# Performance work log

Measured on AMD Instinct MI355X. Metric: run time of the kernel, lower is better.

## Reference

```python
import jax, jax.numpy as jnp
import numpy as np

B, T, H, P = 512, 256, 256, 14  # batch, seq_len, hidden_size, predict_seq


def _lstm_layer(x_tbf, w_ih, w_hh, b_ih, b_hh):
    """One LSTM layer. x_tbf: [T, B, F]. Returns outputs [T, B, H].
    PyTorch gate order: i, f, g, o."""
    # Precompute input contribution for all timesteps: [T, B, 4H]
    pre = jnp.einsum('tbf,gf->tbg', x_tbf, w_ih) + b_ih + b_hh
    h0 = jnp.zeros((x_tbf.shape[1], w_hh.shape[1]), dtype=x_tbf.dtype)
    c0 = jnp.zeros_like(h0)

    def step(carry, pre_t):
        h, c = carry
        gates = pre_t + h @ w_hh.T                      # [B, 4H]
        i, f, g, o = jnp.split(gates, 4, axis=-1)
        i = jax.nn.sigmoid(i)
        f = jax.nn.sigmoid(f)
        g = jnp.tanh(g)
        o = jax.nn.sigmoid(o)
        c = f * c + i * g
        h = o * jnp.tanh(c)
        return (h, c), h

    _, ys = jax.lax.scan(step, (h0, c0), pre)
    return ys  # [T, B, H]


def setup_inputs() -> dict:
    key = jax.random.key(0)
    ks = jax.random.split(key, 11)
    s = 1.0 / np.sqrt(H)  # torch LSTM/Linear default init scale
    return {
        'x':     jax.random.normal(ks[0], (B, T, 1), dtype=jnp.float32),
        'w_ih0': jax.random.uniform(ks[1], (4 * H, 1), jnp.float32, -s, s),
        'w_hh0': jax.random.uniform(ks[2], (4 * H, H), jnp.float32, -s, s),
        'b_ih0': jax.random.uniform(ks[3], (4 * H,), jnp.float32, -s, s),
        'b_hh0': jax.random.uniform(ks[4], (4 * H,), jnp.float32, -s, s),
        'w_ih1': jax.random.uniform(ks[5], (4 * H, H), jnp.float32, -s, s),
        'w_hh1': jax.random.uniform(ks[6], (4 * H, H), jnp.float32, -s, s),
        'b_ih1': jax.random.uniform(ks[7], (4 * H,), jnp.float32, -s, s),
        'b_hh1': jax.random.uniform(ks[8], (4 * H,), jnp.float32, -s, s),
        'w_lin': jax.random.uniform(ks[9], (P, H), jnp.float32, -s, s),
        'b_lin': jax.random.uniform(ks[10], (P,), jnp.float32, -s, s),
    }


def reference(x, w_ih0, w_hh0, b_ih0, b_hh0, w_ih1, w_hh1, b_ih1, b_hh1,
              w_lin, b_lin):
    xt = jnp.transpose(x, (1, 0, 2))                 # [T, B, 1]
    h1 = _lstm_layer(xt, w_ih0, w_hh0, b_ih0, b_hh0)  # [T, B, H]
    h2 = _lstm_layer(h1, w_ih1, w_hh1, b_ih1, b_hh1)  # [T, B, H]
    last = h2[-1]                                     # [B, H] == x[:, -1, :]
    return last @ w_lin.T + b_lin                     # [B, P]
```

## Files before the change

kernel.cpp:

```cpp
#include <hip/hip_runtime.h>

constexpr int Bz = 512;
constexpr int Tz = 256;
constexpr int Hz = 256;
constexpr int Pz = 14;
constexpr int GB = 32;
constexpr int GS = 8;
constexpr int BT = 16;
constexpr int KP = 264;
constexpr int XS = 260;

typedef short s8v __attribute__((ext_vector_type(8)));
typedef float f4v __attribute__((ext_vector_type(4)));
typedef unsigned long long u64;

__device__ __forceinline__ short f2bf(float f) {
  unsigned u = __float_as_uint(f);
  u = (u + 0x7fffu + ((u >> 16) & 1u)) >> 16;
  return (short)u;
}
__device__ __forceinline__ float bf2f(short s) {
  return __uint_as_float(((unsigned)(unsigned short)s) << 16);
}
__device__ __forceinline__ float sigm(float v) {
  return __builtin_amdgcn_rcpf(1.0f + __builtin_amdgcn_exp2f(-1.442695041f * v));
}
__device__ __forceinline__ float tanh_f(float v) {
  return 1.0f - 2.0f * __builtin_amdgcn_rcpf(__builtin_amdgcn_exp2f(2.885390082f * v) + 1.0f);
}

__device__ __forceinline__ u64 llc_load64(const u64* p) {
  return __hip_atomic_load(p, __ATOMIC_RELAXED, __HIP_MEMORY_SCOPE_AGENT);
}
__device__ __forceinline__ unsigned llc_load32(const unsigned* p) {
  return __hip_atomic_load(p, __ATOMIC_RELAXED, __HIP_MEMORY_SCOPE_AGENT);
}
__device__ __forceinline__ void llc_store32(unsigned* p, unsigned v) {
  __hip_atomic_store(p, v, __ATOMIC_RELAXED, __HIP_MEMORY_SCOPE_AGENT);
}
__device__ __forceinline__ void llc_store64(u64* p, u64 v) {
  __hip_atomic_store(p, v, __ATOMIC_RELAXED, __HIP_MEMORY_SCOPE_AGENT);
}

__global__ void __launch_bounds__(256, 1)
lstm2(const float* __restrict__ x,
      const float* __restrict__ w_ih0, const float* __restrict__ w_hh0,
      const float* __restrict__ b_ih0, const float* __restrict__ b_hh0,
      const float* __restrict__ w_ih1, const float* __restrict__ w_hh1,
      const float* __restrict__ b_ih1, const float* __restrict__ b_hh1,
      const float* __restrict__ w_lin, const float* __restrict__ b_lin,
      float* __restrict__ out,
      u64* __restrict__ hg, unsigned* __restrict__ flags)
{
  const int blk  = blockIdx.x;
  const int g    = blk >> 3;
  const int sl   = blk & 7;
  const int tid  = threadIdx.x;
  const int w    = tid >> 6;
  const int lane = tid & 63;
  const int q    = lane >> 4;
  const int l15  = lane & 15;
  const int gbase = g * BT;

  extern __shared__ char smem_raw[];
  short* h0s = (short*)smem_raw;
  short* h1s = h0s + BT * KP;
  float* xls = (float*)(h1s + BT * KP);
  float* wls = xls + BT * XS;

  s8v Wf[3][2][8];
  {
    const float* wsrc[3] = {w_hh0, w_ih1, w_hh1};
    #pragma unroll
    for (int mat = 0; mat < 3; ++mat) {
      #pragma unroll
      for (int mti = 0; mti < 2; ++mti) {
        int rr = (w + mti * 4) * 16 + l15;
        int grow = (rr & 3) * Hz + sl * 32 + (rr >> 2);
        const float* p = wsrc[mat] + (size_t)grow * Hz;
        #pragma unroll
        for (int kt = 0; kt < 8; ++kt) {
          s8v f;
          #pragma unroll
          for (int j = 0; j < 8; ++j) {
            int ktrue = kt * 32 + q * 4 + (j >> 1) + 16 * (j & 1);
            f[j] = f2bf(p[ktrue]);
          }
          Wf[mat][mti][kt] = f;
        }
      }
    }
  }
  const int uA = w * 4 + q, uB = 16 + w * 4 + q;
  float wihA[4], wihB[4], b0A[4], b0B[4], b1A[4], b1B[4];
  #pragma unroll
  for (int r = 0; r < 4; ++r) {
    int ga_ = r * Hz + sl * 32 + uA;
    int gb_ = r * Hz + sl * 32 + uB;
    wihA[r] = w_ih0[ga_];              wihB[r] = w_ih0[gb_];
    b0A[r]  = b_ih0[ga_] + b_hh0[ga_]; b0B[r]  = b_ih0[gb_] + b_hh0[gb_];
    b1A[r]  = b_ih1[ga_] + b_hh1[ga_]; b1B[r]  = b_ih1[gb_] + b_hh1[gb_];
  }
  float c0A = 0.f, c0B = 0.f, c1A = 0.f, c1B = 0.f;

  for (int i = tid; i < BT * (Tz / 4); i += 256) {
    int b = i >> 6, c4 = i & 63;
    f4v v = *(const f4v*)(x + (size_t)(gbase + b) * Tz + c4 * 4);
    *(f4v*)(xls + b * XS + c4 * 4) = v;
  }
  if (sl == 0) {
    for (int i = tid; i < Pz * Hz; i += 256) {
      int p = i >> 8, kpos = i & 255;
      int sl2 = kpos >> 5, w2 = (kpos >> 3) & 3, q2 = (kpos >> 1) & 3, jj = kpos & 1;
      wls[i] = w_lin[p * Hz + sl2 * 32 + w2 * 4 + q2 + 16 * jj];
    }
  }

  const unsigned* myflags = flags + g * 32 + (lane & 7);
  unsigned* myflag = flags + g * 32 + sl;

  for (int s = 0; s <= Tz; ++s) {
    if (w == 0) {
      const unsigned expd = (unsigned)s;
      unsigned f = llc_load32(myflags);
      while (__ballot(f >= expd) != ~0ull) {
        __builtin_amdgcn_s_sleep(1);
        f = llc_load32(myflags);
      }
    }
    __syncthreads();

    {
      const u64* sp = hg + (size_t)((s + 1) & 1) * 65536;
      u64 r[8];
      #pragma unroll
      for (int k = 0; k < 4; ++k) {
        int i = tid + k * 256;
        int c = i & 1, b = (i >> 1) & 15, slw = i >> 5;
        size_t gi = ((size_t)slw * Bz + gbase + b) * 4 + 2 * c;
        r[2 * k]     = llc_load64(sp + gi);
        r[2 * k + 1] = llc_load64(sp + gi + 1);
      }
      #pragma unroll
      for (int k = 0; k < 4; ++k) {
        int i = tid + k * 256;
        int c = i & 1, b = (i >> 1) & 15, slw = i >> 5;
        u64 lo = r[2 * k], hi = r[2 * k + 1];
        *(u64*)(h0s + b * KP + slw * 8 + c * 4) =
            (u64)(unsigned)lo | ((u64)(unsigned)hi << 32);
        *(u64*)(h1s + b * KP + slw * 8 + c * 4) =
            (lo >> 32) | ((hi >> 32) << 32);
      }
    }
    __syncthreads();

    f4v a0A = {0.f,0.f,0.f,0.f}, a0B = {0.f,0.f,0.f,0.f};
    f4v a1A = {0.f,0.f,0.f,0.f}, a1B = {0.f,0.f,0.f,0.f};
    const short* H0f = h0s + l15 * KP + q * 8;
    const short* H1f = h1s + l15 * KP + q * 8;
    #pragma unroll
    for (int kt = 0; kt < 8; ++kt) {
      s8v h0v = *(const s8v*)(H0f + kt * 32);
      s8v h1v = *(const s8v*)(H1f + kt * 32);
      a0A = __builtin_amdgcn_mfma_f32_16x16x32_bf16(Wf[0][0][kt], h0v, a0A, 0, 0, 0);
      a0B = __builtin_amdgcn_mfma_f32_16x16x32_bf16(Wf[0][1][kt], h0v, a0B, 0, 0, 0);
      a1A = __builtin_amdgcn_mfma_f32_16x16x32_bf16(Wf[1][0][kt], h0v, a1A, 0, 0, 0);
      a1B = __builtin_amdgcn_mfma_f32_16x16x32_bf16(Wf[1][1][kt], h0v, a1B, 0, 0, 0);
      a1A = __builtin_amdgcn_mfma_f32_16x16x32_bf16(Wf[2][0][kt], h1v, a1A, 0, 0, 0);
      a1B = __builtin_amdgcn_mfma_f32_16x16x32_bf16(Wf[2][1][kt], h1v, a1B, 0, 0, 0);
    }

    unsigned pk0 = 0, pk1 = 0;
    if (s < Tz) {
      float xv = xls[l15 * XS + s];
      float iA = sigm  (a0A[0] + xv * wihA[0] + b0A[0]);
      float fA = sigm  (a0A[1] + xv * wihA[1] + b0A[1]);
      float gA = tanh_f(a0A[2] + xv * wihA[2] + b0A[2]);
      float oA = sigm  (a0A[3] + xv * wihA[3] + b0A[3]);
      c0A = fA * c0A + iA * gA;
      float iB = sigm  (a0B[0] + xv * wihB[0] + b0B[0]);
      float fB = sigm  (a0B[1] + xv * wihB[1] + b0B[1]);
      float gB = tanh_f(a0B[2] + xv * wihB[2] + b0B[2]);
      float oB = sigm  (a0B[3] + xv * wihB[3] + b0B[3]);
      c0B = fB * c0B + iB * gB;
      pk0 = (unsigned)(unsigned short)f2bf(oA * tanh_f(c0A))
          | ((unsigned)(unsigned short)f2bf(oB * tanh_f(c0B)) << 16);
    }
    if (s >= 1) {
      float iA = sigm  (a1A[0] + b1A[0]);
      float fA = sigm  (a1A[1] + b1A[1]);
      float gA = tanh_f(a1A[2] + b1A[2]);
      float oA = sigm  (a1A[3] + b1A[3]);
      c1A = fA * c1A + iA * gA;
      float iB = sigm  (a1B[0] + b1B[0]);
      float fB = sigm  (a1B[1] + b1B[1]);
      float gB = tanh_f(a1B[2] + b1B[2]);
      float oB = sigm  (a1B[3] + b1B[3]);
      c1B = fB * c1B + iB * gB;
      pk1 = (unsigned)(unsigned short)f2bf(oA * tanh_f(c1A))
          | ((unsigned)(unsigned short)f2bf(oB * tanh_f(c1B)) << 16);
    }

    {
      size_t base = (size_t)(sl * 4 + w) * 2048 + (size_t)(gbase + l15) * 4 + q;
      llc_store64(hg + (size_t)(s & 1) * 65536 + base,
                  (u64)pk0 | ((u64)pk1 << 32));
    }

    __syncthreads();
    if (tid == 0)
      llc_store32(myflag, (unsigned)(s + 1));
  }

  if (sl == 0) {
    {
      const unsigned expd = (unsigned)(Tz + 1);
      unsigned f = llc_load32(myflags);
      while (__ballot(f >= expd) != ~0ull) {
        __builtin_amdgcn_s_sleep(1);
        f = llc_load32(myflags);
      }
    }
    const u64* sp = hg + (size_t)(Tz & 1) * 65536;
    for (int k = 0; k < 4; ++k) {
      int i = tid + k * 256;
      int c = i & 1, b = (i >> 1) & 15, slw = i >> 5;
      size_t gi = ((size_t)slw * Bz + gbase + b) * 4 + 2 * c;
      u64 lo = llc_load64(sp + gi);
      u64 hi = llc_load64(sp + gi + 1);
      *(u64*)(h0s + b * KP + slw * 8 + c * 4) = (lo >> 32) | ((hi >> 32) << 32);
    }
    __syncthreads();
    for (int i = tid; i < BT * Pz; i += 256) {
      int b = i / Pz, p = i - b * Pz;
      const float* wr = wls + p * Hz;
      float acc = b_lin[p];
      for (int kk = 0; kk < Hz; ++kk)
        acc += bf2f(h0s[b * KP + kk]) * wr[kk];
      out[(gbase + b) * Pz + p] = acc;
    }
  }
}

extern "C" void kernel_launch(void* const* d_in, const int* in_sizes, int n_in,
                              void* d_out, int out_size, void* d_ws, size_t ws_size,
                              hipStream_t stream) {
  const float* x     = (const float*)d_in[0];
  const float* w_ih0 = (const float*)d_in[1];
  const float* w_hh0 = (const float*)d_in[2];
  const float* b_ih0 = (const float*)d_in[3];
  const float* b_hh0 = (const float*)d_in[4];
  const float* w_ih1 = (const float*)d_in[5];
  const float* w_hh1 = (const float*)d_in[6];
  const float* b_ih1 = (const float*)d_in[7];
  const float* b_hh1 = (const float*)d_in[8];
  const float* w_lin = (const float*)d_in[9];
  const float* b_lin = (const float*)d_in[10];
  float* out = (float*)d_out;

  unsigned char* ws = (unsigned char*)d_ws;
  u64* hg         = (u64*)ws;
  unsigned* flags = (unsigned*)(ws + (1 << 20));
  hipMemsetAsync(d_ws, 0, (1 << 20) + 4096, stream);

  size_t lds_bytes = (size_t)(2 * BT) * KP * 2
                   + (size_t)(BT * XS) * 4
                   + (size_t)(Pz * Hz) * 4;
  hipFuncSetAttribute((const void*)lstm2,
                      hipFuncAttributeMaxDynamicSharedMemorySize, (int)lds_bytes);
  lstm2<<<GB * GS, 256, lds_bytes, stream>>>(x, w_ih0, w_hh0, b_ih0, b_hh0,
                                             w_ih1, w_hh1, b_ih1, b_hh1,
                                             w_lin, b_lin, out, hg, flags);
}
```

Before: 727.5 us.

## Split each batch group across 4 blocks of 512 threads instead of 8

Halves the number of blocks cooperating on each 16-row batch group, from 8 to 4, and doubles threads per block to 512 so each block owns 64 hidden units. Weight fragment indexing, hidden-state exchange layout, flag polling and the final linear weight permutation are remapped to match. The aim is to cut the cross-block flag synchronisation and global hidden-state exchange per timestep, at the cost of more work per block and higher register pressure at 512 threads.

```diff
diff --git a/kernel.cpp b/kernel.cpp
--- a/kernel.cpp
+++ b/kernel.cpp
@@ -5,10 +5,11 @@
 constexpr int Hz = 256;
 constexpr int Pz = 14;
 constexpr int GB = 32;
-constexpr int GS = 8;
+constexpr int GS = 4;
 constexpr int BT = 16;
 constexpr int KP = 264;
 constexpr int XS = 260;
+constexpr int THR = 512;
 
 typedef short s8v __attribute__((ext_vector_type(8)));
 typedef float f4v __attribute__((ext_vector_type(4)));
@@ -42,7 +43,7 @@
   __hip_atomic_store(p, v, __ATOMIC_RELAXED, __HIP_MEMORY_SCOPE_AGENT);
 }
 
-__global__ void __launch_bounds__(256, 1)
+__global__ void __launch_bounds__(512, 1)
 lstm2(const float* __restrict__ x,
       const float* __restrict__ w_ih0, const float* __restrict__ w_hh0,
       const float* __restrict__ b_ih0, const float* __restrict__ b_hh0,
@@ -53,8 +54,8 @@
       u64* __restrict__ hg, unsigned* __restrict__ flags)
 {
   const int blk  = blockIdx.x;
-  const int g    = blk >> 3;
-  const int sl   = blk & 7;
+  const int g    = blk >> 2;
+  const int sl   = blk & 3;
   const int tid  = threadIdx.x;
   const int w    = tid >> 6;
   const int lane = tid & 63;
@@ -75,15 +76,16 @@
     for (int mat = 0; mat < 3; ++mat) {
       #pragma unroll
       for (int mti = 0; mti < 2; ++mti) {
-        int rr = (w + mti * 4) * 16 + l15;
-        int grow = (rr & 3) * Hz + sl * 32 + (rr >> 2);
+        int rr = (w + mti * 8) * 16 + l15;
+        int grow = (rr & 3) * Hz + sl * 64 + (rr >> 2);
         const float* p = wsrc[mat] + (size_t)grow * Hz;
         #pragma unroll
         for (int kt = 0; kt < 8; ++kt) {
           s8v f;
           #pragma unroll
           for (int j = 0; j < 8; ++j) {
-            int ktrue = kt * 32 + q * 4 + (j >> 1) + 16 * (j & 1);
+            int xk = kt * 4 + q;
+            int ktrue = (xk >> 3) * 64 + (xk & 7) * 4 + (j >> 1) + 32 * (j & 1);
             f[j] = f2bf(p[ktrue]);
           }
           Wf[mat][mti][kt] = f;
@@ -91,32 +93,34 @@
       }
     }
   }
-  const int uA = w * 4 + q, uB = 16 + w * 4 + q;
+  const int uA = sl * 64 + w * 4 + q, uB = uA + 32;
   float wihA[4], wihB[4], b0A[4], b0B[4], b1A[4], b1B[4];
   #pragma unroll
   for (int r = 0; r < 4; ++r) {
-    int ga_ = r * Hz + sl * 32 + uA;
-    int gb_ = r * Hz + sl * 32 + uB;
+    int ga_ = r * Hz + uA;
+    int gb_ = r * Hz + uB;
     wihA[r] = w_ih0[ga_];              wihB[r] = w_ih0[gb_];
     b0A[r]  = b_ih0[ga_] + b_hh0[ga_]; b0B[r]  = b_ih0[gb_] + b_hh0[gb_];
     b1A[r]  = b_ih1[ga_] + b_hh1[ga_]; b1B[r]  = b_ih1[gb_] + b_hh1[gb_];
   }
   float c0A = 0.f, c0B = 0.f, c1A = 0.f, c1B = 0.f;
 
-  for (int i = tid; i < BT * (Tz / 4); i += 256) {
+  for (int i = tid; i < BT * (Tz / 4); i += THR) {
     int b = i >> 6, c4 = i & 63;
     f4v v = *(const f4v*)(x + (size_t)(gbase + b) * Tz + c4 * 4);
     *(f4v*)(xls + b * XS + c4 * 4) = v;
   }
   if (sl == 0) {
-    for (int i = tid; i < Pz * Hz; i += 256) {
+    for (int i = tid; i < Pz * Hz; i += THR) {
       int p = i >> 8, kpos = i & 255;
-      int sl2 = kpos >> 5, w2 = (kpos >> 3) & 3, q2 = (kpos >> 1) & 3, jj = kpos & 1;
-      wls[i] = w_lin[p * Hz + sl2 * 32 + w2 * 4 + q2 + 16 * jj];
-    }
-  }
-
-  const unsigned* myflags = flags + g * 32 + (lane & 7);
+      int slw2 = kpos >> 3, inner = kpos & 7;
+      int q2 = inner >> 1, j2 = inner & 1;
+      int ktrue = (slw2 >> 3) * 64 + (slw2 & 7) * 4 + q2 + 32 * j2;
+      wls[i] = w_lin[p * Hz + ktrue];
+    }
+  }
+
+  const unsigned* myflags = flags + g * 32 + (lane & 3);
   unsigned* myflag = flags + g * 32 + sl;
 
   for (int s = 0; s <= Tz; ++s) {
@@ -132,18 +136,18 @@
 
     {
       const u64* sp = hg + (size_t)((s + 1) & 1) * 65536;
-      u64 r[8];
+      u64 r[4];
       #pragma unroll
-      for (int k = 0; k < 4; ++k) {
-        int i = tid + k * 256;
+      for (int k = 0; k < 2; ++k) {
+        int i = tid + k * THR;
         int c = i & 1, b = (i >> 1) & 15, slw = i >> 5;
         size_t gi = ((size_t)slw * Bz + gbase + b) * 4 + 2 * c;
         r[2 * k]     = llc_load64(sp + gi);
         r[2 * k + 1] = llc_load64(sp + gi + 1);
       }
       #pragma unroll
-      for (int k = 0; k < 4; ++k) {
-        int i = tid + k * 256;
+      for (int k = 0; k < 2; ++k) {
+        int i = tid + k * THR;
         int c = i & 1, b = (i >> 1) & 15, slw = i >> 5;
         u64 lo = r[2 * k], hi = r[2 * k + 1];
         *(u64*)(h0s + b * KP + slw * 8 + c * 4) =
@@ -202,7 +206,7 @@
     }
 
     {
-      size_t base = (size_t)(sl * 4 + w) * 2048 + (size_t)(gbase + l15) * 4 + q;
+      size_t base = (size_t)(sl * 8 + w) * 2048 + (size_t)(gbase + l15) * 4 + q;
       llc_store64(hg + (size_t)(s & 1) * 65536 + base,
                   (u64)pk0 | ((u64)pk1 << 32));
     }
@@ -222,8 +226,8 @@
       }
     }
     const u64* sp = hg + (size_t)(Tz & 1) * 65536;
-    for (int k = 0; k < 4; ++k) {
-      int i = tid + k * 256;
+    for (int k = 0; k < 2; ++k) {
+      int i = tid + k * THR;
       int c = i & 1, b = (i >> 1) & 15, slw = i >> 5;
       size_t gi = ((size_t)slw * Bz + gbase + b) * 4 + 2 * c;
       u64 lo = llc_load64(sp + gi);
@@ -231,7 +235,7 @@
       *(u64*)(h0s + b * KP + slw * 8 + c * 4) = (lo >> 32) | ((hi >> 32) << 32);
     }
     __syncthreads();
-    for (int i = tid; i < BT * Pz; i += 256) {
+    for (int i = tid; i < BT * Pz; i += THR) {
       int b = i / Pz, p = i - b * Pz;
       const float* wr = wls + p * Hz;
       float acc = b_lin[p];
@@ -268,7 +272,7 @@
                    + (size_t)(Pz * Hz) * 4;
   hipFuncSetAttribute((const void*)lstm2,
                       hipFuncAttributeMaxDynamicSharedMemorySize, (int)lds_bytes);
-  lstm2<<<GB * GS, 256, lds_bytes, stream>>>(x, w_ih0, w_hh0, b_ih0, b_hh0,
+  lstm2<<<GB * GS, THR, lds_bytes, stream>>>(x, w_ih0, w_hh0, b_ih0, b_hh0,
                                              w_ih1, w_hh1, b_ih1, b_hh1,
                                              w_lin, b_lin, out, hg, flags);
 }
```

Result: slower. 1.098 ms (+51.0%).

## Replace end-of-step block barrier with per-wave atomic counters and double-buffered LDS

Applied to the files above, without the earlier changes.

Drops the trailing __syncthreads and single-thread flag store at the end of each timestep. Each wave now drains its own stores and atomically increments a per-block counter, and waiters expect 4 increments per step. The hidden-state LDS staging is double-buffered by step parity, so a fast wave cannot overwrite data a slower wave is still reading. The intent is to cut one block-wide barrier per step on the latency-bound recurrent path, at the cost of 4x more atomic traffic to the flag lines and twice the LDS for h staging.

```diff
diff --git a/kernel.cpp b/kernel.cpp
--- a/kernel.cpp
+++ b/kernel.cpp
@@ -9,6 +9,7 @@
 constexpr int BT = 16;
 constexpr int KP = 264;
 constexpr int XS = 260;
+constexpr int HBsz = BT * KP;
 
 typedef short s8v __attribute__((ext_vector_type(8)));
 typedef float f4v __attribute__((ext_vector_type(4)));
@@ -34,9 +35,6 @@
 }
 __device__ __forceinline__ unsigned llc_load32(const unsigned* p) {
   return __hip_atomic_load(p, __ATOMIC_RELAXED, __HIP_MEMORY_SCOPE_AGENT);
-}
-__device__ __forceinline__ void llc_store32(unsigned* p, unsigned v) {
-  __hip_atomic_store(p, v, __ATOMIC_RELAXED, __HIP_MEMORY_SCOPE_AGENT);
 }
 __device__ __forceinline__ void llc_store64(u64* p, u64 v) {
   __hip_atomic_store(p, v, __ATOMIC_RELAXED, __HIP_MEMORY_SCOPE_AGENT);
@@ -63,9 +61,8 @@
   const int gbase = g * BT;
 
   extern __shared__ char smem_raw[];
-  short* h0s = (short*)smem_raw;
-  short* h1s = h0s + BT * KP;
-  float* xls = (float*)(h1s + BT * KP);
+  short* hstage = (short*)smem_raw;
+  float* xls = (float*)(hstage + 4 * HBsz);
   float* wls = xls + BT * XS;
 
   s8v Wf[3][2][8];
@@ -116,39 +113,44 @@
     }
   }
 
-  const unsigned* myflags = flags + g * 32 + (lane & 7);
-  unsigned* myflag = flags + g * 32 + sl;
+  const unsigned* myctrs = flags + g * 16 + (lane & 7);
+  unsigned* myctr = flags + g * 16 + sl;
+
+  int cc[4], bb[4], ss[4];
+  #pragma unroll
+  for (int k = 0; k < 4; ++k) {
+    int i = tid + k * 256;
+    cc[k] = i & 1; bb[k] = (i >> 1) & 15; ss[k] = i >> 5;
+  }
 
   for (int s = 0; s <= Tz; ++s) {
     if (w == 0) {
-      const unsigned expd = (unsigned)s;
-      unsigned f = llc_load32(myflags);
+      const unsigned expd = 4u * (unsigned)s;
+      unsigned f = llc_load32(myctrs);
       while (__ballot(f >= expd) != ~0ull) {
         __builtin_amdgcn_s_sleep(1);
-        f = llc_load32(myflags);
+        f = llc_load32(myctrs);
       }
     }
     __syncthreads();
 
+    short* hb0 = hstage + (s & 1) * (2 * HBsz);
+    short* hb1 = hb0 + HBsz;
     {
       const u64* sp = hg + (size_t)((s + 1) & 1) * 65536;
       u64 r[8];
       #pragma unroll
       for (int k = 0; k < 4; ++k) {
-        int i = tid + k * 256;
-        int c = i & 1, b = (i >> 1) & 15, slw = i >> 5;
-        size_t gi = ((size_t)slw * Bz + gbase + b) * 4 + 2 * c;
+        size_t gi = ((size_t)ss[k] * Bz + gbase + bb[k]) * 4 + 2 * cc[k];
         r[2 * k]     = llc_load64(sp + gi);
         r[2 * k + 1] = llc_load64(sp + gi + 1);
       }
       #pragma unroll
       for (int k = 0; k < 4; ++k) {
-        int i = tid + k * 256;
-        int c = i & 1, b = (i >> 1) & 15, slw = i >> 5;
         u64 lo = r[2 * k], hi = r[2 * k + 1];
-        *(u64*)(h0s + b * KP + slw * 8 + c * 4) =
+        *(u64*)(hb0 + bb[k] * KP + ss[k] * 8 + cc[k] * 4) =
             (u64)(unsigned)lo | ((u64)(unsigned)hi << 32);
-        *(u64*)(h1s + b * KP + slw * 8 + c * 4) =
+        *(u64*)(hb1 + bb[k] * KP + ss[k] * 8 + cc[k] * 4) =
             (lo >> 32) | ((hi >> 32) << 32);
       }
     }
@@ -156,8 +158,8 @@
 
     f4v a0A = {0.f,0.f,0.f,0.f}, a0B = {0.f,0.f,0.f,0.f};
     f4v a1A = {0.f,0.f,0.f,0.f}, a1B = {0.f,0.f,0.f,0.f};
-    const short* H0f = h0s + l15 * KP + q * 8;
-    const short* H1f = h1s + l15 * KP + q * 8;
+    const short* H0f = hb0 + l15 * KP + q * 8;
+    const short* H1f = hb1 + l15 * KP + q * 8;
     #pragma unroll
     for (int kt = 0; kt < 8; ++kt) {
       s8v h0v = *(const s8v*)(H0f + kt * 32);
@@ -207,28 +209,30 @@
                   (u64)pk0 | ((u64)pk1 << 32));
     }
 
-    __syncthreads();
-    if (tid == 0)
-      llc_store32(myflag, (unsigned)(s + 1));
+    asm volatile("s_waitcnt vmcnt(0)" ::: "memory");
+    __builtin_amdgcn_sched_barrier(0);
+    if (lane == 0)
+      __hip_atomic_fetch_add(myctr, 1u, __ATOMIC_RELAXED,
+                             __HIP_MEMORY_SCOPE_AGENT);
   }
 
   if (sl == 0) {
     {
-      const unsigned expd = (unsigned)(Tz + 1);
-      unsigned f = llc_load32(myflags);
+      const unsigned expd = 4u * (unsigned)(Tz + 1);
+      unsigned f = llc_load32(myctrs);
       while (__ballot(f >= expd) != ~0ull) {
         __builtin_amdgcn_s_sleep(1);
-        f = llc_load32(myflags);
-      }
-    }
+        f = llc_load32(myctrs);
+      }
+    }
+    short* hb = hstage + 1 * (2 * HBsz);
     const u64* sp = hg + (size_t)(Tz & 1) * 65536;
     for (int k = 0; k < 4; ++k) {
-      int i = tid + k * 256;
-      int c = i & 1, b = (i >> 1) & 15, slw = i >> 5;
-      size_t gi = ((size_t)slw * Bz + gbase + b) * 4 + 2 * c;
+      size_t gi = ((size_t)ss[k] * Bz + gbase + bb[k]) * 4 + 2 * cc[k];
       u64 lo = llc_load64(sp + gi);
       u64 hi = llc_load64(sp + gi + 1);
-      *(u64*)(h0s + b * KP + slw * 8 + c * 4) = (lo >> 32) | ((hi >> 32) << 32);
+      *(u64*)(hb + bb[k] * KP + ss[k] * 8 + cc[k] * 4) =
+          (lo >> 32) | ((hi >> 32) << 32);
     }
     __syncthreads();
     for (int i = tid; i < BT * Pz; i += 256) {
@@ -236,7 +240,7 @@
       const float* wr = wls + p * Hz;
       float acc = b_lin[p];
       for (int kk = 0; kk < Hz; ++kk)
-        acc += bf2f(h0s[b * KP + kk]) * wr[kk];
+        acc += bf2f(hb[b * KP + kk]) * wr[kk];
       out[(gbase + b) * Pz + p] = acc;
     }
   }
@@ -263,7 +267,7 @@
   unsigned* flags = (unsigned*)(ws + (1 << 20));
   hipMemsetAsync(d_ws, 0, (1 << 20) + 4096, stream);
 
-  size_t lds_bytes = (size_t)(2 * BT) * KP * 2
+  size_t lds_bytes = (size_t)(4 * HBsz) * 2
                    + (size_t)(BT * XS) * 4
                    + (size_t)(Pz * Hz) * 4;
   hipFuncSetAttribute((const void*)lstm2,
```

After: 1.020 ms. 40.2% more time.

## Split LSTM layers into separate producer/consumer block roles with decoupled flags

Applied to the files above, without the earlier changes.

Launches twice as many blocks: role 0 blocks run layer 0 only, role 1 blocks run layer 1 and the final linear. Layer 0 is allowed to run up to three steps ahead using a 4-deep h0 ring buffer, and layer 1 waits on per-step flags. This replaces the lockstep wavefront schedule where each block did both layers per step, and halves the per-block register-resident weights so two blocks can fit per CU. It adds extra flag polling traffic and relies on all 512 blocks being co-resident to avoid deadlock.

```diff
diff --git a/kernel.cpp b/kernel.cpp
--- a/kernel.cpp
+++ b/kernel.cpp
@@ -38,11 +38,8 @@
 __device__ __forceinline__ void llc_store32(unsigned* p, unsigned v) {
   __hip_atomic_store(p, v, __ATOMIC_RELAXED, __HIP_MEMORY_SCOPE_AGENT);
 }
-__device__ __forceinline__ void llc_store64(u64* p, u64 v) {
-  __hip_atomic_store(p, v, __ATOMIC_RELAXED, __HIP_MEMORY_SCOPE_AGENT);
-}
-
-__global__ void __launch_bounds__(256, 1)
+
+__global__ void __launch_bounds__(256, 2)
 lstm2(const float* __restrict__ x,
       const float* __restrict__ w_ih0, const float* __restrict__ w_hh0,
       const float* __restrict__ b_ih0, const float* __restrict__ b_hh0,
@@ -50,11 +47,14 @@
       const float* __restrict__ b_ih1, const float* __restrict__ b_hh1,
       const float* __restrict__ w_lin, const float* __restrict__ b_lin,
       float* __restrict__ out,
-      u64* __restrict__ hg, unsigned* __restrict__ flags)
+      unsigned* __restrict__ h0g, unsigned* __restrict__ h1g,
+      unsigned* __restrict__ flags)
 {
   const int blk  = blockIdx.x;
-  const int g    = blk >> 3;
-  const int sl   = blk & 7;
+  const int role = blk >> 8;
+  const int sub  = blk & 255;
+  const int g    = sub >> 3;
+  const int sl   = sub & 7;
   const int tid  = threadIdx.x;
   const int w    = tid >> 6;
   const int lane = tid & 63;
@@ -68,110 +68,84 @@
   float* xls = (float*)(h1s + BT * KP);
   float* wls = xls + BT * XS;
 
-  s8v Wf[3][2][8];
-  {
-    const float* wsrc[3] = {w_hh0, w_ih1, w_hh1};
+  int cc[4], bb[4], ss[4];
+  #pragma unroll
+  for (int k = 0; k < 4; ++k) {
+    int i = tid + k * 256;
+    cc[k] = i & 1; bb[k] = (i >> 1) & 15; ss[k] = i >> 5;
+  }
+  const size_t stbase = (size_t)(sl * 4 + w) * 2048 + (size_t)(gbase + l15) * 4 + q;
+
+  if (role == 0) {
+    s8v Wf0[2][8];
     #pragma unroll
-    for (int mat = 0; mat < 3; ++mat) {
+    for (int mti = 0; mti < 2; ++mti) {
+      int rr = (w + mti * 4) * 16 + l15;
+      int grow = (rr & 3) * Hz + sl * 32 + (rr >> 2);
+      const float* p = w_hh0 + (size_t)grow * Hz;
       #pragma unroll
-      for (int mti = 0; mti < 2; ++mti) {
-        int rr = (w + mti * 4) * 16 + l15;
-        int grow = (rr & 3) * Hz + sl * 32 + (rr >> 2);
-        const float* p = wsrc[mat] + (size_t)grow * Hz;
-        #pragma unroll
-        for (int kt = 0; kt < 8; ++kt) {
-          s8v f;
-          #pragma unroll
-          for (int j = 0; j < 8; ++j) {
-            int ktrue = kt * 32 + q * 4 + (j >> 1) + 16 * (j & 1);
-            f[j] = f2bf(p[ktrue]);
-          }
-          Wf[mat][mti][kt] = f;
-        }
-      }
-    }
-  }
-  const int uA = w * 4 + q, uB = 16 + w * 4 + q;
-  float wihA[4], wihB[4], b0A[4], b0B[4], b1A[4], b1B[4];
-  #pragma unroll
-  for (int r = 0; r < 4; ++r) {
-    int ga_ = r * Hz + sl * 32 + uA;
-    int gb_ = r * Hz + sl * 32 + uB;
-    wihA[r] = w_ih0[ga_];              wihB[r] = w_ih0[gb_];
-    b0A[r]  = b_ih0[ga_] + b_hh0[ga_]; b0B[r]  = b_ih0[gb_] + b_hh0[gb_];
-    b1A[r]  = b_ih1[ga_] + b_hh1[ga_]; b1B[r]  = b_ih1[gb_] + b_hh1[gb_];
-  }
-  float c0A = 0.f, c0B = 0.f, c1A = 0.f, c1B = 0.f;
-
-  for (int i = tid; i < BT * (Tz / 4); i += 256) {
-    int b = i >> 6, c4 = i & 63;
-    f4v v = *(const f4v*)(x + (size_t)(gbase + b) * Tz + c4 * 4);
-    *(f4v*)(xls + b * XS + c4 * 4) = v;
-  }
-  if (sl == 0) {
-    for (int i = tid; i < Pz * Hz; i += 256) {
-      int p = i >> 8, kpos = i & 255;
-      int sl2 = kpos >> 5, w2 = (kpos >> 3) & 3, q2 = (kpos >> 1) & 3, jj = kpos & 1;
-      wls[i] = w_lin[p * Hz + sl2 * 32 + w2 * 4 + q2 + 16 * jj];
-    }
-  }
-
-  const unsigned* myflags = flags + g * 32 + (lane & 7);
-  unsigned* myflag = flags + g * 32 + sl;
-
-  for (int s = 0; s <= Tz; ++s) {
-    if (w == 0) {
-      const unsigned expd = (unsigned)s;
-      unsigned f = llc_load32(myflags);
-      while (__ballot(f >= expd) != ~0ull) {
-        __builtin_amdgcn_s_sleep(1);
-        f = llc_load32(myflags);
-      }
-    }
-    __syncthreads();
-
-    {
-      const u64* sp = hg + (size_t)((s + 1) & 1) * 65536;
-      u64 r[8];
+      for (int kt = 0; kt < 8; ++kt) {
+        s8v f;
+        #pragma unroll
+        for (int j = 0; j < 8; ++j) {
+          int ktrue = kt * 32 + q * 4 + (j >> 1) + 16 * (j & 1);
+          f[j] = f2bf(p[ktrue]);
+        }
+        Wf0[mti][kt] = f;
+      }
+    }
+    const int uA = w * 4 + q, uB = 16 + w * 4 + q;
+    float wihA[4], wihB[4], b0A[4], b0B[4];
+    #pragma unroll
+    for (int r = 0; r < 4; ++r) {
+      int ga_ = r * Hz + sl * 32 + uA;
+      int gb_ = r * Hz + sl * 32 + uB;
+      wihA[r] = w_ih0[ga_];              wihB[r] = w_ih0[gb_];
+      b0A[r]  = b_ih0[ga_] + b_hh0[ga_]; b0B[r]  = b_ih0[gb_] + b_hh0[gb_];
+    }
+    float c0A = 0.f, c0B = 0.f;
+
+    for (int i = tid; i < BT * (Tz / 4); i += 256) {
+      int b = i >> 6, c4 = i & 63;
+      f4v v = *(const f4v*)(x + (size_t)(gbase + b) * Tz + c4 * 4);
+      *(f4v*)(xls + b * XS + c4 * 4) = v;
+    }
+
+    for (int s = 0; s < Tz; ++s) {
+      if (w == 0) {
+        const unsigned lf = lane & 15;
+        const unsigned e = (lf < 8) ? (unsigned)s
+                                    : (unsigned)(s >= 3 ? s - 3 : 0);
+        const unsigned* fp = flags + g * 32 + lf;
+        unsigned f = llc_load32(fp);
+        while (__ballot(f >= e) != ~0ull) {
+          __builtin_amdgcn_s_sleep(1);
+          f = llc_load32(fp);
+        }
+      }
+      __syncthreads();
+
+      {
+        const u64* sp = (const u64*)h0g + (size_t)((s - 1) & 3) * 32768;
+        u64 r[4];
+        #pragma unroll
+        for (int k = 0; k < 4; ++k)
+          r[k] = llc_load64(sp + ((size_t)ss[k] * Bz + gbase + bb[k]) * 2 + cc[k]);
+        #pragma unroll
+        for (int k = 0; k < 4; ++k)
+          *(u64*)(h0s + bb[k] * KP + ss[k] * 8 + cc[k] * 4) = r[k];
+      }
+      __syncthreads();
+
+      f4v a0A = {0.f,0.f,0.f,0.f}, a0B = {0.f,0.f,0.f,0.f};
+      const short* H0f = h0s + l15 * KP + q * 8;
       #pragma unroll
-      for (int k = 0; k < 4; ++k) {
-        int i = tid + k * 256;
-        int c = i & 1, b = (i >> 1) & 15, slw = i >> 5;
-        size_t gi = ((size_t)slw * Bz + gbase + b) * 4 + 2 * c;
-        r[2 * k]     = llc_load64(sp + gi);
-        r[2 * k + 1] = llc_load64(sp + gi + 1);
-      }
-      #pragma unroll
-      for (int k = 0; k < 4; ++k) {
-        int i = tid + k * 256;
-        int c = i & 1, b = (i >> 1) & 15, slw = i >> 5;
-        u64 lo = r[2 * k], hi = r[2 * k + 1];
-        *(u64*)(h0s + b * KP + slw * 8 + c * 4) =
-            (u64)(unsigned)lo | ((u64)(unsigned)hi << 32);
-        *(u64*)(h1s + b * KP + slw * 8 + c * 4) =
-            (lo >> 32) | ((hi >> 32) << 32);
-      }
-    }
-    __syncthreads();
-
-    f4v a0A = {0.f,0.f,0.f,0.f}, a0B = {0.f,0.f,0.f,0.f};
-    f4v a1A = {0.f,0.f,0.f,0.f}, a1B = {0.f,0.f,0.f,0.f};
-    const short* H0f = h0s + l15 * KP + q * 8;
-    const short* H1f = h1s + l15 * KP + q * 8;
-    #pragma unroll
-    for (int kt = 0; kt < 8; ++kt) {
-      s8v h0v = *(const s8v*)(H0f + kt * 32);
-      s8v h1v = *(const s8v*)(H1f + kt * 32);
-      a0A = __builtin_amdgcn_mfma_f32_16x16x32_bf16(Wf[0][0][kt], h0v, a0A, 0, 0, 0);
-      a0B = __builtin_amdgcn_mfma_f32_16x16x32_bf16(Wf[0][1][kt], h0v, a0B, 0, 0, 0);
-      a1A = __builtin_amdgcn_mfma_f32_16x16x32_bf16(Wf[1][0][kt], h0v, a1A, 0, 0, 0);
-      a1B = __builtin_amdgcn_mfma_f32_16x16x32_bf16(Wf[1][1][kt], h0v, a1B, 0, 0, 0);
-      a1A = __builtin_amdgcn_mfma_f32_16x16x32_bf16(Wf[2][0][kt], h1v, a1A, 0, 0, 0);
-      a1B = __builtin_amdgcn_mfma_f32_16x16x32_bf16(Wf[2][1][kt], h1v, a1B, 0, 0, 0);
-    }
-
-    unsigned pk0 = 0, pk1 = 0;
-    if (s < Tz) {
+      for (int kt = 0; kt < 8; ++kt) {
+        s8v h0v = *(const s8v*)(H0f + kt * 32);
+        a0A = __builtin_amdgcn_mfma_f32_16x16x32_bf16(Wf0[0][kt], h0v, a0A, 0, 0, 0);
+        a0B = __builtin_amdgcn_mfma_f32_16x16x32_bf16(Wf0[1][kt], h0v, a0B, 0, 0, 0);
+      }
+
       float xv = xls[l15 * XS + s];
       float iA = sigm  (a0A[0] + xv * wihA[0] + b0A[0]);
       float fA = sigm  (a0A[1] + xv * wihA[1] + b0A[1]);
@@ -183,10 +157,102 @@
       float gB = tanh_f(a0B[2] + xv * wihB[2] + b0B[2]);
       float oB = sigm  (a0B[3] + xv * wihB[3] + b0B[3]);
       c0B = fB * c0B + iB * gB;
-      pk0 = (unsigned)(unsigned short)f2bf(oA * tanh_f(c0A))
-          | ((unsigned)(unsigned short)f2bf(oB * tanh_f(c0B)) << 16);
-    }
-    if (s >= 1) {
+      unsigned pk0 = (unsigned)(unsigned short)f2bf(oA * tanh_f(c0A))
+                   | ((unsigned)(unsigned short)f2bf(oB * tanh_f(c0B)) << 16);
+
+      llc_store32(h0g + (size_t)(s & 3) * 65536 + stbase, pk0);
+
+      __syncthreads();
+      if (tid == 0)
+        llc_store32(flags + g * 32 + sl, (unsigned)(s + 1));
+    }
+  } else {
+    s8v Wf[2][2][8];
+    {
+      const float* wsrc[2] = {w_ih1, w_hh1};
+      #pragma unroll
+      for (int mat = 0; mat < 2; ++mat) {
+        #pragma unroll
+        for (int mti = 0; mti < 2; ++mti) {
+          int rr = (w + mti * 4) * 16 + l15;
+          int grow = (rr & 3) * Hz + sl * 32 + (rr >> 2);
+          const float* p = wsrc[mat] + (size_t)grow * Hz;
+          #pragma unroll
+          for (int kt = 0; kt < 8; ++kt) {
+            s8v f;
+            #pragma unroll
+            for (int j = 0; j < 8; ++j) {
+              int ktrue = kt * 32 + q * 4 + (j >> 1) + 16 * (j & 1);
+              f[j] = f2bf(p[ktrue]);
+            }
+            Wf[mat][mti][kt] = f;
+          }
+        }
+      }
+    }
+    const int uA = w * 4 + q, uB = 16 + w * 4 + q;
+    float b1A[4], b1B[4];
+    #pragma unroll
+    for (int r = 0; r < 4; ++r) {
+      int ga_ = r * Hz + sl * 32 + uA;
+      int gb_ = r * Hz + sl * 32 + uB;
+      b1A[r] = b_ih1[ga_] + b_hh1[ga_];
+      b1B[r] = b_ih1[gb_] + b_hh1[gb_];
+    }
+    float c1A = 0.f, c1B = 0.f;
+
+    if (sl == 0) {
+      for (int i = tid; i < Pz * Hz; i += 256) {
+        int p = i >> 8, kpos = i & 255;
+        int sl2 = kpos >> 5, w2 = (kpos >> 3) & 3, q2 = (kpos >> 1) & 3, jj = kpos & 1;
+        wls[i] = w_lin[p * Hz + sl2 * 32 + w2 * 4 + q2 + 16 * jj];
+      }
+    }
+
+    for (int t = 0; t < Tz; ++t) {
+      if (w == 0) {
+        const unsigned lf = lane & 15;
+        const unsigned e = (lf < 8) ? (unsigned)(t + 1) : (unsigned)t;
+        const unsigned* fp = flags + g * 32 + lf;
+        unsigned f = llc_load32(fp);
+        while (__ballot(f >= e) != ~0ull) {
+          __builtin_amdgcn_s_sleep(1);
+          f = llc_load32(fp);
+        }
+      }
+      __syncthreads();
+
+      {
+        const u64* sp0 = (const u64*)h0g + (size_t)(t & 3) * 32768;
+        const u64* sp1 = (const u64*)h1g + (size_t)((t - 1) & 1) * 32768;
+        u64 r0[4], r1[4];
+        #pragma unroll
+        for (int k = 0; k < 4; ++k) {
+          size_t gi = ((size_t)ss[k] * Bz + gbase + bb[k]) * 2 + cc[k];
+          r0[k] = llc_load64(sp0 + gi);
+          r1[k] = llc_load64(sp1 + gi);
+        }
+        #pragma unroll
+        for (int k = 0; k < 4; ++k) {
+          *(u64*)(h0s + bb[k] * KP + ss[k] * 8 + cc[k] * 4) = r0[k];
+          *(u64*)(h1s + bb[k] * KP + ss[k] * 8 + cc[k] * 4) = r1[k];
+        }
+      }
+      __syncthreads();
+
+      f4v a1A = {0.f,0.f,0.f,0.f}, a1B = {0.f,0.f,0.f,0.f};
+      const short* H0f = h0s + l15 * KP + q * 8;
+      const short* H1f = h1s + l15 * KP + q * 8;
+      #pragma unroll
+      for (int kt = 0; kt < 8; ++kt) {
+        s8v h0v = *(const s8v*)(H0f + kt * 32);
+        s8v h1v = *(const s8v*)(H1f + kt * 32);
+        a1A = __builtin_amdgcn_mfma_f32_16x16x32_bf16(Wf[0][0][kt], h0v, a1A, 0, 0, 0);
+        a1B = __builtin_amdgcn_mfma_f32_16x16x32_bf16(Wf[0][1][kt], h0v, a1B, 0, 0, 0);
+        a1A = __builtin_amdgcn_mfma_f32_16x16x32_bf16(Wf[1][0][kt], h1v, a1A, 0, 0, 0);
+        a1B = __builtin_amdgcn_mfma_f32_16x16x32_bf16(Wf[1][1][kt], h1v, a1B, 0, 0, 0);
+      }
+
       float iA = sigm  (a1A[0] + b1A[0]);
       float fA = sigm  (a1A[1] + b1A[1]);
       float gA = tanh_f(a1A[2] + b1A[2]);
@@ -197,47 +263,40 @@
       float gB = tanh_f(a1B[2] + b1B[2]);
       float oB = sigm  (a1B[3] + b1B[3]);
       c1B = fB * c1B + iB * gB;
-      pk1 = (unsigned)(unsigned short)f2bf(oA * tanh_f(c1A))
-          | ((unsigned)(unsigned short)f2bf(oB * tanh_f(c1B)) << 16);
-    }
-
-    {
-      size_t base = (size_t)(sl * 4 + w) * 2048 + (size_t)(gbase + l15) * 4 + q;
-      llc_store64(hg + (size_t)(s & 1) * 65536 + base,
-                  (u64)pk0 | ((u64)pk1 << 32));
-    }
-
-    __syncthreads();
-    if (tid == 0)
-      llc_store32(myflag, (unsigned)(s + 1));
-  }
-
-  if (sl == 0) {
-    {
-      const unsigned expd = (unsigned)(Tz + 1);
-      unsigned f = llc_load32(myflags);
-      while (__ballot(f >= expd) != ~0ull) {
-        __builtin_amdgcn_s_sleep(1);
-        f = llc_load32(myflags);
-      }
-    }
-    const u64* sp = hg + (size_t)(Tz & 1) * 65536;
-    for (int k = 0; k < 4; ++k) {
-      int i = tid + k * 256;
-      int c = i & 1, b = (i >> 1) & 15, slw = i >> 5;
-      size_t gi = ((size_t)slw * Bz + gbase + b) * 4 + 2 * c;
-      u64 lo = llc_load64(sp + gi);
-      u64 hi = llc_load64(sp + gi + 1);
-      *(u64*)(h0s + b * KP + slw * 8 + c * 4) = (lo >> 32) | ((hi >> 32) << 32);
-    }
-    __syncthreads();
-    for (int i = tid; i < BT * Pz; i += 256) {
-      int b = i / Pz, p = i - b * Pz;
-      const float* wr = wls + p * Hz;
-      float acc = b_lin[p];
-      for (int kk = 0; kk < Hz; ++kk)
-        acc += bf2f(h0s[b * KP + kk]) * wr[kk];
-      out[(gbase + b) * Pz + p] = acc;
+      unsigned pk1 = (unsigned)(unsigned short)f2bf(oA * tanh_f(c1A))
+                   | ((unsigned)(unsigned short)f2bf(oB * tanh_f(c1B)) << 16);
+
+      llc_store32(h1g + (size_t)(t & 1) * 65536 + stbase, pk1);
+
+      __syncthreads();
+      if (tid == 0)
+        llc_store32(flags + g * 32 + 8 + sl, (unsigned)(t + 1));
+    }
+
+    if (sl == 0) {
+      {
+        const unsigned expd = (unsigned)Tz;
+        const unsigned* fp = flags + g * 32 + 8 + (lane & 7);
+        unsigned f = llc_load32(fp);
+        while (__ballot(f >= expd) != ~0ull) {
+          __builtin_amdgcn_s_sleep(1);
+          f = llc_load32(fp);
+        }
+      }
+      const u64* sp = (const u64*)h1g + (size_t)((Tz - 1) & 1) * 32768;
+      for (int k = 0; k < 4; ++k) {
+        u64 v = llc_load64(sp + ((size_t)ss[k] * Bz + gbase + bb[k]) * 2 + cc[k]);
+        *(u64*)(h0s + bb[k] * KP + ss[k] * 8 + cc[k] * 4) = v;
+      }
+      __syncthreads();
+      for (int i = tid; i < BT * Pz; i += 256) {
+        int b = i / Pz, p = i - b * Pz;
+        const float* wr = wls + p * Hz;
+        float acc = b_lin[p];
+        for (int kk = 0; kk < Hz; ++kk)
+          acc += bf2f(h0s[b * KP + kk]) * wr[kk];
+        out[(gbase + b) * Pz + p] = acc;
+      }
     }
   }
 }
@@ -259,16 +318,17 @@
   float* out = (float*)d_out;
 
   unsigned char* ws = (unsigned char*)d_ws;
-  u64* hg         = (u64*)ws;
-  unsigned* flags = (unsigned*)(ws + (1 << 20));
-  hipMemsetAsync(d_ws, 0, (1 << 20) + 4096, stream);
+  unsigned* h0g   = (unsigned*)ws;
+  unsigned* h1g   = (unsigned*)(ws + (1 << 20));
+  unsigned* flags = (unsigned*)(ws + (1536 << 10));
+  hipMemsetAsync(d_ws, 0, (1536 << 10) + 4096, stream);
 
   size_t lds_bytes = (size_t)(2 * BT) * KP * 2
                    + (size_t)(BT * XS) * 4
                    + (size_t)(Pz * Hz) * 4;
   hipFuncSetAttribute((const void*)lstm2,
                       hipFuncAttributeMaxDynamicSharedMemorySize, (int)lds_bytes);
-  lstm2<<<GB * GS, 256, lds_bytes, stream>>>(x, w_ih0, w_hh0, b_ih0, b_hh0,
-                                             w_ih1, w_hh1, b_ih1, b_hh1,
-                                             w_lin, b_lin, out, hg, flags);
-}
+  lstm2<<<2 * GB * GS, 256, lds_bytes, stream>>>(x, w_ih0, w_hh0, b_ih0, b_hh0,
+                                                 w_ih1, w_hh1, b_ih1, b_hh1,
+                                                 w_lin, b_lin, out, h0g, h1g, flags);
+}
```

New measurement: 859.6 us. 18.2% more time.
